# Optimization experiments

Hardware: AMD Instinct MI355X
Metric: run time of the kernel (lower is better)

## Reference

```python
import jax, jax.numpy as jnp
import numpy as np

D_EEG_MAX = 10.0
H_FMRI_MAX = 5.0
CLZ_MAX = 3.0
D_MAX = 1.0  # config.diffusion_coefficient_range[1]
N_LEVELS = 8  # discretization levels -> 64 pair-histogram bins


def setup_inputs() -> dict:
    key = jax.random.key(0)
    k1, k2 = jax.random.split(key)
    B, E = 8192, 4096
    psi_distribution = jax.random.uniform(k1, (B, E), dtype=jnp.float32)
    fractal_field = jax.random.normal(k2, (B, E), dtype=jnp.float32)
    fci_weights = jnp.array([0.4, 0.3, 0.3], dtype=jnp.float32)
    return {"psi_distribution": psi_distribution,
            "fractal_field": fractal_field,
            "fci_weights": fci_weights}


def _d_eeg(psi):
    # entropy of P(psi) per row, averaged; torch.std is unbiased (ddof=1)
    entropy = -jnp.sum(psi * jnp.log(psi + 1e-10), axis=-1).mean()
    spatial_variation = jnp.std(psi, axis=-1, ddof=1).mean()
    return jnp.minimum(entropy * spatial_variation * 3.0, D_EEG_MAX)


def _spatial_correlation(field):
    # Pearson corr between adjacent feature columns over the batch, vectorized
    c = field - field.mean(axis=0, keepdims=True)          # [B, E]
    var = jnp.sum(c * c, axis=0)                            # [E]
    cov = jnp.sum(c[:, :-1] * c[:, 1:], axis=0)             # [E-1]
    corr = cov / jnp.sqrt(var[:-1] * var[1:])               # [E-1]
    mask = ~jnp.isnan(corr)                                 # torch code skips NaNs
    n = jnp.sum(mask)
    mean_corr = jnp.where(n > 0,
                          jnp.sum(jnp.where(mask, corr, 0.0)) / jnp.maximum(n, 1),
                          0.0)
    return jnp.abs(mean_corr)


def _h_fmri(field):
    field_magnitude = jnp.linalg.norm(field, axis=-1).mean()
    correlation = _spatial_correlation(field)
    return jnp.minimum(field_magnitude * correlation * 2.0, H_FMRI_MAX)


def _conditional_entropy(psi):
    # discretize to 8 levels; count (curr,next) pairs with a 64-bin histogram
    q = jnp.clip(jnp.floor(psi * N_LEVELS), 0, N_LEVELS - 1).astype(jnp.int32)  # [B, E]
    pair_ids = (q[:, :-1] * N_LEVELS + q[:, 1:]).reshape(-1)                    # [B*(E-1)]
    counts = jnp.zeros((N_LEVELS * N_LEVELS,), jnp.float32).at[pair_ids].add(1.0)
    total = pair_ids.shape[0]  # static
    p = counts / total
    return -jnp.sum(jnp.where(p > 0, p * jnp.log2(jnp.where(p > 0, p, 1.0)), 0.0))


def _clz(psi, field):
    cond_ent = _conditional_entropy(psi)
    field_complexity = jnp.std(field, ddof=1)  # torch.std over all elems, unbiased
    return jnp.minimum(cond_ent + 0.3 * field_complexity, CLZ_MAX)


def reference(psi_distribution, fractal_field, fci_weights):
    d_eeg = _d_eeg(psi_distribution)
    h_fmri = _h_fmri(fractal_field)
    clz = _clz(psi_distribution, fractal_field)
    fci_num = (fci_weights[0] * (d_eeg / D_EEG_MAX)
               + fci_weights[1] * (h_fmri / H_FMRI_MAX)
               + fci_weights[2] * (clz / CLZ_MAX))
    return jnp.clip(fci_num / D_MAX, 0.0, 1.0)
```

## Files before the change

kernel.cpp:

```cpp
#include <hip/hip_runtime.h>
#include <math.h>

#define BATCH 8192
#define EDIM  4096
#define NBINS 64
#define NGRP  128
#define ROWSW (BATCH / NGRP)
#define NCHK  16
#define NREP_FB 64

#define OFF_HISTP   0u
#define OFF_CSP     (2u * 1024 * 1024 / 4)
#define OFF_CQP     (4u * 1024 * 1024 / 4)
#define OFF_PPP     (6u * 1024 * 1024 / 4)
#define OFF_RFSQP   (8u * 1024 * 1024 / 4)
#define OFF_ROWENT  (OFF_RFSQP + NCHK * BATCH)
#define OFF_ROWSTD  (OFF_ROWENT + BATCH)
#define OFF_ROWFSQ  (OFF_ROWSTD + BATCH)
#define OFF_COLSUM  (OFF_ROWFSQ + BATCH)
#define OFF_COLSQ   (OFF_COLSUM + EDIM)
#define OFF_PAIRP   (OFF_COLSQ + EDIM)
#define OFF_HIST2   (OFF_PAIRP + EDIM)
#define PRIMARY_WS_BYTES ((OFF_HIST2 + 2 * NBINS) * 4)


__global__ __launch_bounds__(256) void psi_pass(const float* __restrict__ psi,
                                                unsigned* __restrict__ hist,
                                                float* __restrict__ row_ent,
                                                float* __restrict__ row_std,
                                                int fb) {
  const int r = blockIdx.x;
  const int t = threadIdx.x;
  const float4* row = (const float4*)(psi + (size_t)r * EDIM);

  __shared__ unsigned lhist[NBINS];
  __shared__ float firsts[EDIM / 4];
  __shared__ float red[12];

  if (t < NBINS) lhist[t] = 0u;

  float4 v[4];
#pragma unroll
  for (int k = 0; k < 4; ++k) v[k] = row[t + k * 256];
#pragma unroll
  for (int k = 0; k < 4; ++k) firsts[t + k * 256] = v[k].x;
  __syncthreads();

  float s = 0.f, sq = 0.f, pl = 0.f;
#pragma unroll
  for (int k = 0; k < 4; ++k) {
    const int vi = t + k * 256;
    float ee[4] = {v[k].x, v[k].y, v[k].z, v[k].w};
    int q[4];
#pragma unroll
    for (int j = 0; j < 4; ++j) {
      float x = ee[j];
      s += x;
      sq += x * x;
      pl += x * __logf(x + 1e-10f);
      int qq = (int)floorf(x * 8.0f);
      q[j] = min(max(qq, 0), 7);
    }
#pragma unroll
    for (int j = 0; j < 3; ++j)
      atomicAdd(&lhist[q[j] * 8 + q[j + 1]], 1u);
    if (vi < EDIM / 4 - 1) {
      float xn = firsts[vi + 1];
      int qn = min(max((int)floorf(xn * 8.0f), 0), 7);
      atomicAdd(&lhist[q[3] * 8 + qn], 1u);
    }
  }

  for (int off = 32; off; off >>= 1) {
    s  += __shfl_down(s, off);
    sq += __shfl_down(sq, off);
    pl += __shfl_down(pl, off);
  }
  const int w = t >> 6, lane = t & 63;
  if (lane == 0) { red[w] = s; red[4 + w] = sq; red[8 + w] = pl; }
  __syncthreads();
  if (t == 0) {
    float S  = red[0] + red[1] + red[2] + red[3];
    float SQ = red[4] + red[5] + red[6] + red[7];
    float PL = red[8] + red[9] + red[10] + red[11];
    row_ent[r] = -PL;
    float var = (SQ - S * S / (float)EDIM) / (float)(EDIM - 1);
    row_std[r] = sqrtf(fmaxf(var, 0.f));
  }
  if (t < NBINS) {
    if (fb) atomicAdd(&hist[(size_t)(r & (NREP_FB - 1)) * NBINS + t], lhist[t]);
    else    hist[(size_t)r * NBINS + t] = lhist[t];
  }
}

__global__ __launch_bounds__(256) void field_pass(const float* __restrict__ f,
                                                  float* __restrict__ cs_part,
                                                  float* __restrict__ cq_part,
                                                  float* __restrict__ pp_part,
                                                  float* __restrict__ rfsq_part) {
  const int gw = (blockIdx.x * 256 + threadIdx.x) >> 6;
  const int lane = threadIdx.x & 63;
  const int cchunk = gw & (NCHK - 1);
  const int g = gw >> 4;
  const int c0 = cchunk * 256 + lane * 4;
  const int r0 = g * ROWSW;

  float cs0 = 0.f, cs1 = 0.f, cs2 = 0.f, cs3 = 0.f;
  float cq0 = 0.f, cq1 = 0.f, cq2 = 0.f, cq3 = 0.f;
  float pp0 = 0.f, pp1 = 0.f, pp2 = 0.f, pp3 = 0.f;
#pragma unroll 8
  for (int i = 0; i < ROWSW; ++i) {
    const int r = r0 + i;
    const float4 v = *(const float4*)(f + (size_t)r * EDIM + c0);
    cs0 += v.x; cs1 += v.y; cs2 += v.z; cs3 += v.w;
    cq0 = fmaf(v.x, v.x, cq0); cq1 = fmaf(v.y, v.y, cq1);
    cq2 = fmaf(v.z, v.z, cq2); cq3 = fmaf(v.w, v.w, cq3);
    pp0 = fmaf(v.x, v.y, pp0); pp1 = fmaf(v.y, v.z, pp1); pp2 = fmaf(v.z, v.w, pp2);
    float nx = __shfl_down(v.x, 1);
    if (lane != 63) pp3 = fmaf(v.w, nx, pp3);
    float rs = fmaf(v.x, v.x, fmaf(v.y, v.y, fmaf(v.z, v.z, v.w * v.w)));
    for (int off = 32; off; off >>= 1) rs += __shfl_down(rs, off);
    if (lane == 0) rfsq_part[(size_t)cchunk * BATCH + r] = rs;
  }
  const size_t cb = (size_t)g * EDIM + c0;
  *(float4*)(cs_part + cb) = make_float4(cs0, cs1, cs2, cs3);
  *(float4*)(cq_part + cb) = make_float4(cq0, cq1, cq2, cq3);
  *(float4*)(pp_part + cb) = make_float4(pp0, pp1, pp2, pp3);
}

__global__ __launch_bounds__(256) void field_pass_fb(const float* __restrict__ f,
                                                     float* __restrict__ colsum,
                                                     float* __restrict__ colsumsq,
                                                     float* __restrict__ pairprod,
                                                     float* __restrict__ row_fsq) {
  const int gw = (blockIdx.x * 256 + threadIdx.x) >> 6;
  const int lane = threadIdx.x & 63;
  const int cchunk = gw & 15;
  const int rgroup = gw >> 4;
  const int c0 = cchunk * 256 + lane * 4;
  const int r0 = rgroup * (BATCH / 512);

  float cs0 = 0.f, cs1 = 0.f, cs2 = 0.f, cs3 = 0.f;
  float cq0 = 0.f, cq1 = 0.f, cq2 = 0.f, cq3 = 0.f;
  float pp0 = 0.f, pp1 = 0.f, pp2 = 0.f, pp3 = 0.f;
#pragma unroll 8
  for (int i = 0; i < BATCH / 512; ++i) {
    const int r = r0 + i;
    const float4 v = *(const float4*)(f + (size_t)r * EDIM + c0);
    cs0 += v.x; cs1 += v.y; cs2 += v.z; cs3 += v.w;
    cq0 = fmaf(v.x, v.x, cq0); cq1 = fmaf(v.y, v.y, cq1);
    cq2 = fmaf(v.z, v.z, cq2); cq3 = fmaf(v.w, v.w, cq3);
    pp0 = fmaf(v.x, v.y, pp0); pp1 = fmaf(v.y, v.z, pp1); pp2 = fmaf(v.z, v.w, pp2);
    float nx = __shfl_down(v.x, 1);
    if (lane != 63) pp3 = fmaf(v.w, nx, pp3);
    float rs = fmaf(v.x, v.x, fmaf(v.y, v.y, fmaf(v.z, v.z, v.w * v.w)));
    for (int off = 32; off; off >>= 1) rs += __shfl_down(rs, off);
    if (lane == 0) atomicAdd(&row_fsq[r], rs);
  }
  atomicAdd(&colsum[c0 + 0], cs0);  atomicAdd(&colsumsq[c0 + 0], cq0);
  atomicAdd(&colsum[c0 + 1], cs1);  atomicAdd(&colsumsq[c0 + 1], cq1);
  atomicAdd(&colsum[c0 + 2], cs2);  atomicAdd(&colsumsq[c0 + 2], cq2);
  atomicAdd(&colsum[c0 + 3], cs3);  atomicAdd(&colsumsq[c0 + 3], cq3);
  atomicAdd(&pairprod[c0 + 0], pp0);
  atomicAdd(&pairprod[c0 + 1], pp1);
  atomicAdd(&pairprod[c0 + 2], pp2);
  if (lane != 63) atomicAdd(&pairprod[c0 + 3], pp3);
}

__global__ __launch_bounds__(256) void boundary_pass(const float* __restrict__ f,
                                                     float* __restrict__ pairprod) {
  __shared__ float sred[4];
  const int c = blockIdx.x * 256 + 255;
  const int t = threadIdx.x;
  float acc = 0.f;
  for (int r = t; r < BATCH; r += 256)
    acc = fmaf(f[(size_t)r * EDIM + c], f[(size_t)r * EDIM + c + 1], acc);
  for (int off = 32; off; off >>= 1) acc += __shfl_down(acc, off);
  if ((t & 63) == 0) sred[t >> 6] = acc;
  __syncthreads();
  if (t == 0) pairprod[c] = sred[0] + sred[1] + sred[2] + sred[3];
}

__global__ __launch_bounds__(256) void reduce_pass(const float* __restrict__ f,
                                                   const unsigned* __restrict__ hist_part,
                                                   const float* __restrict__ cs_part,
                                                   const float* __restrict__ cq_part,
                                                   const float* __restrict__ pp_part,
                                                   const float* __restrict__ rfsq_part,
                                                   float* __restrict__ colsum,
                                                   float* __restrict__ colsumsq,
                                                   float* __restrict__ pairprod,
                                                   float* __restrict__ row_fsq,
                                                   unsigned* __restrict__ hist2) {
  const int b = blockIdx.x;
  const int t = threadIdx.x;

  if (b < 48) {
    const int stat = b >> 4;
    const int c = (b & 15) * 256 + t;
    const float* part = (stat == 0) ? cs_part : (stat == 1) ? cq_part : pp_part;
    float acc = 0.f;
#pragma unroll 8
    for (int g = 0; g < NGRP; ++g) acc += part[(size_t)g * EDIM + c];
    if (stat == 0) colsum[c] = acc;
    else if (stat == 1) colsumsq[c] = acc;
    else if ((c & 255) != 255) pairprod[c] = acc;
  } else if (b < 80) {
    const int r = (b - 48) * 256 + t;
    float acc = 0.f;
#pragma unroll
    for (int k = 0; k < NCHK; ++k) acc += rfsq_part[(size_t)k * BATCH + r];
    row_fsq[r] = acc;
  } else if (b < 88) {
    __shared__ unsigned hred[4][NBINS];
    const int j = b - 80;
    const int bin = t & 63, quad = t >> 6;
    unsigned acc = 0u;
    for (int pb = j * 1024 + quad; pb < (j + 1) * 1024; pb += 4)
      acc += hist_part[(size_t)pb * NBINS + bin];
    hred[quad][bin] = acc;
    __syncthreads();
    if (t < NBINS)
      hist2[(size_t)j * NBINS + t] = hred[0][t] + hred[1][t] + hred[2][t] + hred[3][t];
  } else {
    __shared__ float sred[4];
    const int c = (b - 88) * 256 + 255;
    float acc = 0.f;
    for (int r = t; r < BATCH; r += 256)
      acc = fmaf(f[(size_t)r * EDIM + c], f[(size_t)r * EDIM + c + 1], acc);
    for (int off = 32; off; off >>= 1) acc += __shfl_down(acc, off);
    if ((t & 63) == 0) sred[t >> 6] = acc;
    __syncthreads();
    if (t == 0) pairprod[c] = sred[0] + sred[1] + sred[2] + sred[3];
  }
}

__device__ double blk_reduce(double v, double* sbuf) {
  const int t = threadIdx.x;
  for (int off = 32; off; off >>= 1) v += __shfl_down(v, off);
  __syncthreads();
  if ((t & 63) == 0) sbuf[t >> 6] = v;
  __syncthreads();
  return sbuf[0] + sbuf[1] + sbuf[2] + sbuf[3];
}

__global__ __launch_bounds__(256) void finalize(const unsigned* __restrict__ hist,
                                                int nreps,
                                                const float* __restrict__ row_ent,
                                                const float* __restrict__ row_std,
                                                const float* __restrict__ row_fsq,
                                                const float* __restrict__ colsum,
                                                const float* __restrict__ colsumsq,
                                                const float* __restrict__ pairprod,
                                                const float* __restrict__ wts,
                                                float* __restrict__ out) {
  const int t = threadIdx.x;
  __shared__ double sbuf[4];

  double se = 0, ss = 0, sm = 0;
  for (int i = t; i < BATCH; i += 256) {
    se += (double)row_ent[i];
    ss += (double)row_std[i];
    sm += (double)sqrtf(row_fsq[i]);
  }
  double SE = blk_reduce(se, sbuf);
  double SS = blk_reduce(ss, sbuf);
  double SM = blk_reduce(sm, sbuf);

  double csum = 0, ccnt = 0;
  for (int e = t; e < EDIM - 1; e += 256) {
    double sa = colsum[e], sb = colsum[e + 1];
    double va = (double)colsumsq[e]     - sa * sa / (double)BATCH;
    double vb = (double)colsumsq[e + 1] - sb * sb / (double)BATCH;
    double cov = (double)pairprod[e] - sa * sb / (double)BATCH;
    double corr = cov / sqrt(va * vb);
    if (!isnan(corr)) { csum += corr; ccnt += 1.0; }
  }
  double CS = blk_reduce(csum, sbuf);
  double CN = blk_reduce(ccnt, sbuf);

  double gs = 0, gq = 0;
  for (int e = t; e < EDIM; e += 256) { gs += (double)colsum[e]; gq += (double)colsumsq[e]; }
  double GS = blk_reduce(gs, sbuf);
  double GQ = blk_reduce(gq, sbuf);

  double hent = 0;
  if (t < NBINS) {
    unsigned long long cnt = 0;
    for (int j = 0; j < nreps; ++j) cnt += (unsigned long long)hist[(size_t)j * NBINS + t];
    const double total = (double)BATCH * (double)(EDIM - 1);
    double p = (double)cnt / total;
    if (p > 0.0) hent = -p * log2(p);
  }
  double HE = blk_reduce(hent, sbuf);

  if (t == 0) {
    double entropy = SE / (double)BATCH;
    double spat = SS / (double)BATCH;
    double d_eeg = fmin(entropy * spat * 3.0, 10.0);

    double mag = SM / (double)BATCH;
    double mean_corr = (CN > 0.0) ? (CS / CN) : 0.0;
    double h_fmri = fmin(mag * fabs(mean_corr) * 2.0, 5.0);

    double Nf = (double)BATCH * (double)EDIM;
    double gvar = (GQ - GS * GS / Nf) / (Nf - 1.0);
    double fstd = sqrt(fmax(gvar, 0.0));
    double clz = fmin(HE + 0.3 * fstd, 3.0);

    double fci = (double)wts[0] * (d_eeg / 10.0)
               + (double)wts[1] * (h_fmri / 5.0)
               + (double)wts[2] * (clz / 3.0);
    fci = fmin(fmax(fci, 0.0), 1.0);
    out[0] = (float)fci;
  }
}

extern "C" void kernel_launch(void* const* d_in, const int* in_sizes, int n_in,
                              void* d_out, int out_size, void* d_ws, size_t ws_size,
                              hipStream_t stream) {
  const float* psi = (const float*)d_in[0];
  const float* fld = (const float*)d_in[1];
  const float* wts = (const float*)d_in[2];
  float* out = (float*)d_out;
  float* ws = (float*)d_ws;

  if (ws_size >= (size_t)PRIMARY_WS_BYTES) {
    unsigned* hist_part = (unsigned*)(ws + OFF_HISTP);
    float* cs_part   = ws + OFF_CSP;
    float* cq_part   = ws + OFF_CQP;
    float* pp_part   = ws + OFF_PPP;
    float* rfsq_part = ws + OFF_RFSQP;
    float* row_ent   = ws + OFF_ROWENT;
    float* row_std   = ws + OFF_ROWSTD;
    float* row_fsq   = ws + OFF_ROWFSQ;
    float* colsum    = ws + OFF_COLSUM;
    float* colsumsq  = ws + OFF_COLSQ;
    float* pairprod  = ws + OFF_PAIRP;
    unsigned* hist2  = (unsigned*)(ws + OFF_HIST2);

    psi_pass<<<BATCH, 256, 0, stream>>>(psi, hist_part, row_ent, row_std, 0);
    field_pass<<<(NGRP * NCHK) / 4, 256, 0, stream>>>(fld, cs_part, cq_part, pp_part, rfsq_part);
    reduce_pass<<<103, 256, 0, stream>>>(fld, hist_part, cs_part, cq_part, pp_part,
                                         rfsq_part, colsum, colsumsq, pairprod, row_fsq, hist2);
    finalize<<<1, 256, 0, stream>>>(hist2, 8, row_ent, row_std, row_fsq,
                                    colsum, colsumsq, pairprod, wts, out);
  } else {
    char* wb = (char*)d_ws;
    unsigned* ghist = (unsigned*)(wb);
    float* row_ent  = (float*)(wb + 16384);
    float* row_std  = (float*)(wb + 49152);
    float* row_fsq  = (float*)(wb + 81920);
    float* colsum   = (float*)(wb + 114688);
    float* colsumsq = (float*)(wb + 131072);
    float* pairprod = (float*)(wb + 147456);

    hipMemsetAsync(d_ws, 0, 163840, stream);
    psi_pass<<<BATCH, 256, 0, stream>>>(psi, ghist, row_ent, row_std, 1);
    field_pass_fb<<<2048, 256, 0, stream>>>(fld, colsum, colsumsq, pairprod, row_fsq);
    boundary_pass<<<15, 256, 0, stream>>>(fld, pairprod);
    finalize<<<1, 256, 0, stream>>>(ghist, NREP_FB, row_ent, row_std, row_fsq,
                                    colsum, colsumsq, pairprod, wts, out);
  }
}
```

Baseline: 351.8 us.

## Fuse psi and field passes into one interleaved kernel launch

Merges the psi row pass and the field column pass into a single kernel of 8704 blocks. Within each group of 17 blocks, 16 handle psi rows and one handles a field tile. The goal is for the compute-heavy psi work (log, histogram atomics) and the bandwidth-heavy field work to run at the same time, and to save one launch. It also drops the small-workspace fallback path and turns a few accumulations into FMAs. The field blocks are long-running and may leave a tail at the end of the grid. Removing the fallback means the code now assumes the workspace is large enough.

```diff
diff --git a/kernel.cpp b/kernel.cpp
--- a/kernel.cpp
+++ b/kernel.cpp
@@ -7,7 +7,6 @@
 #define NGRP  128
 #define ROWSW (BATCH / NGRP)
 #define NCHK  16
-#define NREP_FB 64
 
 #define OFF_HISTP   0u
 #define OFF_CSP     (2u * 1024 * 1024 / 4)
@@ -21,21 +20,59 @@
 #define OFF_COLSQ   (OFF_COLSUM + EDIM)
 #define OFF_PAIRP   (OFF_COLSQ + EDIM)
 #define OFF_HIST2   (OFF_PAIRP + EDIM)
-#define PRIMARY_WS_BYTES ((OFF_HIST2 + 2 * NBINS) * 4)
-
-
-__global__ __launch_bounds__(256) void psi_pass(const float* __restrict__ psi,
-                                                unsigned* __restrict__ hist,
-                                                float* __restrict__ row_ent,
-                                                float* __restrict__ row_std,
-                                                int fb) {
-  const int r = blockIdx.x;
-  const int t = threadIdx.x;
-  const float4* row = (const float4*)(psi + (size_t)r * EDIM);
+
+__global__ __launch_bounds__(256) void main_pass(const float* __restrict__ psi,
+                                                 const float* __restrict__ f,
+                                                 unsigned* __restrict__ hist_part,
+                                                 float* __restrict__ row_ent,
+                                                 float* __restrict__ row_std,
+                                                 float* __restrict__ cs_part,
+                                                 float* __restrict__ cq_part,
+                                                 float* __restrict__ pp_part,
+                                                 float* __restrict__ rfsq_part) {
+  const int b = blockIdx.x;
+  const int grp = b / 17;
+  const int sub = b - grp * 17;
+  const int t = threadIdx.x;
 
   __shared__ unsigned lhist[NBINS];
   __shared__ float firsts[EDIM / 4];
   __shared__ float red[12];
+
+  if (sub == 16) {
+    const int gw = grp * 4 + (t >> 6);
+    const int lane = t & 63;
+    const int cchunk = gw & (NCHK - 1);
+    const int g = gw >> 4;
+    const int c0 = cchunk * 256 + lane * 4;
+    const int r0 = g * ROWSW;
+
+    float cs0 = 0.f, cs1 = 0.f, cs2 = 0.f, cs3 = 0.f;
+    float cq0 = 0.f, cq1 = 0.f, cq2 = 0.f, cq3 = 0.f;
+    float pp0 = 0.f, pp1 = 0.f, pp2 = 0.f, pp3 = 0.f;
+#pragma unroll 8
+    for (int i = 0; i < ROWSW; ++i) {
+      const int r = r0 + i;
+      const float4 v = *(const float4*)(f + (size_t)r * EDIM + c0);
+      cs0 += v.x; cs1 += v.y; cs2 += v.z; cs3 += v.w;
+      cq0 = fmaf(v.x, v.x, cq0); cq1 = fmaf(v.y, v.y, cq1);
+      cq2 = fmaf(v.z, v.z, cq2); cq3 = fmaf(v.w, v.w, cq3);
+      pp0 = fmaf(v.x, v.y, pp0); pp1 = fmaf(v.y, v.z, pp1); pp2 = fmaf(v.z, v.w, pp2);
+      float nx = __shfl_down(v.x, 1);
+      if (lane != 63) pp3 = fmaf(v.w, nx, pp3);
+      float rs = fmaf(v.x, v.x, fmaf(v.y, v.y, fmaf(v.z, v.z, v.w * v.w)));
+      for (int off = 32; off; off >>= 1) rs += __shfl_down(rs, off);
+      if (lane == 0) rfsq_part[(size_t)cchunk * BATCH + r] = rs;
+    }
+    const size_t cb = (size_t)g * EDIM + c0;
+    *(float4*)(cs_part + cb) = make_float4(cs0, cs1, cs2, cs3);
+    *(float4*)(cq_part + cb) = make_float4(cq0, cq1, cq2, cq3);
+    *(float4*)(pp_part + cb) = make_float4(pp0, pp1, pp2, pp3);
+    return;
+  }
+
+  const int r = grp * 16 + sub;
+  const float4* row = (const float4*)(psi + (size_t)r * EDIM);
 
   if (t < NBINS) lhist[t] = 0u;
 
@@ -56,8 +93,8 @@
     for (int j = 0; j < 4; ++j) {
       float x = ee[j];
       s += x;
-      sq += x * x;
-      pl += x * __logf(x + 1e-10f);
+      sq = fmaf(x, x, sq);
+      pl = fmaf(x, __logf(x + 1e-10f), pl);
       int qq = (int)floorf(x * 8.0f);
       q[j] = min(max(qq, 0), 7);
     }
@@ -87,98 +124,7 @@
     float var = (SQ - S * S / (float)EDIM) / (float)(EDIM - 1);
     row_std[r] = sqrtf(fmaxf(var, 0.f));
   }
-  if (t < NBINS) {
-    if (fb) atomicAdd(&hist[(size_t)(r & (NREP_FB - 1)) * NBINS + t], lhist[t]);
-    else    hist[(size_t)r * NBINS + t] = lhist[t];
-  }
-}
-
-__global__ __launch_bounds__(256) void field_pass(const float* __restrict__ f,
-                                                  float* __restrict__ cs_part,
-                                                  float* __restrict__ cq_part,
-                                                  float* __restrict__ pp_part,
-                                                  float* __restrict__ rfsq_part) {
-  const int gw = (blockIdx.x * 256 + threadIdx.x) >> 6;
-  const int lane = threadIdx.x & 63;
-  const int cchunk = gw & (NCHK - 1);
-  const int g = gw >> 4;
-  const int c0 = cchunk * 256 + lane * 4;
-  const int r0 = g * ROWSW;
-
-  float cs0 = 0.f, cs1 = 0.f, cs2 = 0.f, cs3 = 0.f;
-  float cq0 = 0.f, cq1 = 0.f, cq2 = 0.f, cq3 = 0.f;
-  float pp0 = 0.f, pp1 = 0.f, pp2 = 0.f, pp3 = 0.f;
-#pragma unroll 8
-  for (int i = 0; i < ROWSW; ++i) {
-    const int r = r0 + i;
-    const float4 v = *(const float4*)(f + (size_t)r * EDIM + c0);
-    cs0 += v.x; cs1 += v.y; cs2 += v.z; cs3 += v.w;
-    cq0 = fmaf(v.x, v.x, cq0); cq1 = fmaf(v.y, v.y, cq1);
-    cq2 = fmaf(v.z, v.z, cq2); cq3 = fmaf(v.w, v.w, cq3);
-    pp0 = fmaf(v.x, v.y, pp0); pp1 = fmaf(v.y, v.z, pp1); pp2 = fmaf(v.z, v.w, pp2);
-    float nx = __shfl_down(v.x, 1);
-    if (lane != 63) pp3 = fmaf(v.w, nx, pp3);
-    float rs = fmaf(v.x, v.x, fmaf(v.y, v.y, fmaf(v.z, v.z, v.w * v.w)));
-    for (int off = 32; off; off >>= 1) rs += __shfl_down(rs, off);
-    if (lane == 0) rfsq_part[(size_t)cchunk * BATCH + r] = rs;
-  }
-  const size_t cb = (size_t)g * EDIM + c0;
-  *(float4*)(cs_part + cb) = make_float4(cs0, cs1, cs2, cs3);
-  *(float4*)(cq_part + cb) = make_float4(cq0, cq1, cq2, cq3);
-  *(float4*)(pp_part + cb) = make_float4(pp0, pp1, pp2, pp3);
-}
-
-__global__ __launch_bounds__(256) void field_pass_fb(const float* __restrict__ f,
-                                                     float* __restrict__ colsum,
-                                                     float* __restrict__ colsumsq,
-                                                     float* __restrict__ pairprod,
-                                                     float* __restrict__ row_fsq) {
-  const int gw = (blockIdx.x * 256 + threadIdx.x) >> 6;
-  const int lane = threadIdx.x & 63;
-  const int cchunk = gw & 15;
-  const int rgroup = gw >> 4;
-  const int c0 = cchunk * 256 + lane * 4;
-  const int r0 = rgroup * (BATCH / 512);
-
-  float cs0 = 0.f, cs1 = 0.f, cs2 = 0.f, cs3 = 0.f;
-  float cq0 = 0.f, cq1 = 0.f, cq2 = 0.f, cq3 = 0.f;
-  float pp0 = 0.f, pp1 = 0.f, pp2 = 0.f, pp3 = 0.f;
-#pragma unroll 8
-  for (int i = 0; i < BATCH / 512; ++i) {
-    const int r = r0 + i;
-    const float4 v = *(const float4*)(f + (size_t)r * EDIM + c0);
-    cs0 += v.x; cs1 += v.y; cs2 += v.z; cs3 += v.w;
-    cq0 = fmaf(v.x, v.x, cq0); cq1 = fmaf(v.y, v.y, cq1);
-    cq2 = fmaf(v.z, v.z, cq2); cq3 = fmaf(v.w, v.w, cq3);
-    pp0 = fmaf(v.x, v.y, pp0); pp1 = fmaf(v.y, v.z, pp1); pp2 = fmaf(v.z, v.w, pp2);
-    float nx = __shfl_down(v.x, 1);
-    if (lane != 63) pp3 = fmaf(v.w, nx, pp3);
-    float rs = fmaf(v.x, v.x, fmaf(v.y, v.y, fmaf(v.z, v.z, v.w * v.w)));
-    for (int off = 32; off; off >>= 1) rs += __shfl_down(rs, off);
-    if (lane == 0) atomicAdd(&row_fsq[r], rs);
-  }
-  atomicAdd(&colsum[c0 + 0], cs0);  atomicAdd(&colsumsq[c0 + 0], cq0);
-  atomicAdd(&colsum[c0 + 1], cs1);  atomicAdd(&colsumsq[c0 + 1], cq1);
-  atomicAdd(&colsum[c0 + 2], cs2);  atomicAdd(&colsumsq[c0 + 2], cq2);
-  atomicAdd(&colsum[c0 + 3], cs3);  atomicAdd(&colsumsq[c0 + 3], cq3);
-  atomicAdd(&pairprod[c0 + 0], pp0);
-  atomicAdd(&pairprod[c0 + 1], pp1);
-  atomicAdd(&pairprod[c0 + 2], pp2);
-  if (lane != 63) atomicAdd(&pairprod[c0 + 3], pp3);
-}
-
-__global__ __launch_bounds__(256) void boundary_pass(const float* __restrict__ f,
-                                                     float* __restrict__ pairprod) {
-  __shared__ float sred[4];
-  const int c = blockIdx.x * 256 + 255;
-  const int t = threadIdx.x;
-  float acc = 0.f;
-  for (int r = t; r < BATCH; r += 256)
-    acc = fmaf(f[(size_t)r * EDIM + c], f[(size_t)r * EDIM + c + 1], acc);
-  for (int off = 32; off; off >>= 1) acc += __shfl_down(acc, off);
-  if ((t & 63) == 0) sred[t >> 6] = acc;
-  __syncthreads();
-  if (t == 0) pairprod[c] = sred[0] + sred[1] + sred[2] + sred[3];
+  if (t < NBINS) hist_part[(size_t)r * NBINS + t] = lhist[t];
 }
 
 __global__ __launch_bounds__(256) void reduce_pass(const float* __restrict__ f,
@@ -244,8 +190,7 @@
   return sbuf[0] + sbuf[1] + sbuf[2] + sbuf[3];
 }
 
-__global__ __launch_bounds__(256) void finalize(const unsigned* __restrict__ hist,
-                                                int nreps,
+__global__ __launch_bounds__(256) void finalize(const unsigned* __restrict__ hist2,
                                                 const float* __restrict__ row_ent,
                                                 const float* __restrict__ row_std,
                                                 const float* __restrict__ row_fsq,
@@ -287,7 +232,8 @@
   double hent = 0;
   if (t < NBINS) {
     unsigned long long cnt = 0;
-    for (int j = 0; j < nreps; ++j) cnt += (unsigned long long)hist[(size_t)j * NBINS + t];
+#pragma unroll
+    for (int j = 0; j < 8; ++j) cnt += (unsigned long long)hist2[j * NBINS + t];
     const double total = (double)BATCH * (double)(EDIM - 1);
     double p = (double)cnt / total;
     if (p > 0.0) hent = -p * log2(p);
@@ -325,41 +271,23 @@
   float* out = (float*)d_out;
   float* ws = (float*)d_ws;
 
-  if (ws_size >= (size_t)PRIMARY_WS_BYTES) {
-    unsigned* hist_part = (unsigned*)(ws + OFF_HISTP);
-    float* cs_part   = ws + OFF_CSP;
-    float* cq_part   = ws + OFF_CQP;
-    float* pp_part   = ws + OFF_PPP;
-    float* rfsq_part = ws + OFF_RFSQP;
-    float* row_ent   = ws + OFF_ROWENT;
-    float* row_std   = ws + OFF_ROWSTD;
-    float* row_fsq   = ws + OFF_ROWFSQ;
-    float* colsum    = ws + OFF_COLSUM;
-    float* colsumsq  = ws + OFF_COLSQ;
-    float* pairprod  = ws + OFF_PAIRP;
-    unsigned* hist2  = (unsigned*)(ws + OFF_HIST2);
-
-    psi_pass<<<BATCH, 256, 0, stream>>>(psi, hist_part, row_ent, row_std, 0);
-    field_pass<<<(NGRP * NCHK) / 4, 256, 0, stream>>>(fld, cs_part, cq_part, pp_part, rfsq_part);
-    reduce_pass<<<103, 256, 0, stream>>>(fld, hist_part, cs_part, cq_part, pp_part,
-                                         rfsq_part, colsum, colsumsq, pairprod, row_fsq, hist2);
-    finalize<<<1, 256, 0, stream>>>(hist2, 8, row_ent, row_std, row_fsq,
-                                    colsum, colsumsq, pairprod, wts, out);
-  } else {
-    char* wb = (char*)d_ws;
-    unsigned* ghist = (unsigned*)(wb);
-    float* row_ent  = (float*)(wb + 16384);
-    float* row_std  = (float*)(wb + 49152);
-    float* row_fsq  = (float*)(wb + 81920);
-    float* colsum   = (float*)(wb + 114688);
-    float* colsumsq = (float*)(wb + 131072);
-    float* pairprod = (float*)(wb + 147456);
-
-    hipMemsetAsync(d_ws, 0, 163840, stream);
-    psi_pass<<<BATCH, 256, 0, stream>>>(psi, ghist, row_ent, row_std, 1);
-    field_pass_fb<<<2048, 256, 0, stream>>>(fld, colsum, colsumsq, pairprod, row_fsq);
-    boundary_pass<<<15, 256, 0, stream>>>(fld, pairprod);
-    finalize<<<1, 256, 0, stream>>>(ghist, NREP_FB, row_ent, row_std, row_fsq,
-                                    colsum, colsumsq, pairprod, wts, out);
-  }
-}
+  unsigned* hist_part = (unsigned*)(ws + OFF_HISTP);
+  float* cs_part   = ws + OFF_CSP;
+  float* cq_part   = ws + OFF_CQP;
+  float* pp_part   = ws + OFF_PPP;
+  float* rfsq_part = ws + OFF_RFSQP;
+  float* row_ent   = ws + OFF_ROWENT;
+  float* row_std   = ws + OFF_ROWSTD;
+  float* row_fsq   = ws + OFF_ROWFSQ;
+  float* colsum    = ws + OFF_COLSUM;
+  float* colsumsq  = ws + OFF_COLSQ;
+  float* pairprod  = ws + OFF_PAIRP;
+  unsigned* hist2  = (unsigned*)(ws + OFF_HIST2);
+
+  main_pass<<<8704, 256, 0, stream>>>(psi, fld, hist_part, row_ent, row_std,
+                                      cs_part, cq_part, pp_part, rfsq_part);
+  reduce_pass<<<103, 256, 0, stream>>>(fld, hist_part, cs_part, cq_part, pp_part,
+                                       rfsq_part, colsum, colsumsq, pairprod, row_fsq, hist2);
+  finalize<<<1, 256, 0, stream>>>(hist2, row_ent, row_std, row_fsq,
+                                  colsum, colsumsq, pairprod, wts, out);
+}
```

After: 353.8 us. No clear change (+0.6%).
